# Kernel optimization log

Measured on AMD Instinct MI355X. Metric: run time of the kernel, lower is better.

Reference implementation:

```python
import jax, jax.numpy as jnp
import numpy as np

N_NODES = 2097152  # total nodes
HIDDEN = 64        # feature dim D

def setup_inputs() -> dict:
    key = jax.random.key(0)
    features = jax.random.normal(key, (N_NODES, HIDDEN), dtype=jnp.float32)
    return {"features": features, "n_per_graph": 512}

def reference(features, n_per_graph):
    # features: [N, D]; N = B * n_per_graph (uniform segments)
    N, D = features.shape
    B = N // n_per_graph
    X = features.reshape(B, n_per_graph, D)          # [B, n, D]
    mu = jnp.mean(X, axis=1, keepdims=True)          # [B, 1, D]
    Xc = X - mu                                      # mean-centered
    # per-graph covariance: (Xc^T Xc) / n  -> [B, D, D]
    cov = jnp.einsum('bnd,bne->bde', Xc, Xc) / jnp.asarray(n_per_graph, X.dtype)
    iu0, iu1 = jnp.triu_indices(D)                   # upper triangle incl. diag
    return cov[:, iu0, iu1]                          # [B, D*(D+1)/2]
```

## Files before the change

kernel.cpp:

```cpp
#include <hip/hip_runtime.h>
#include <hip/hip_bf16.h>


#define DD   64
#define NPG  512
#define NIT  (NPG / 32)

typedef __bf16 bf16x8 __attribute__((ext_vector_type(8)));
typedef float  f32x4  __attribute__((ext_vector_type(4)));

__global__ __launch_bounds__(256, 4)
void cov_pool_kernel(const float* __restrict__ X, float* __restrict__ out,
                     int n_graphs) {
  const int lane = threadIdx.x & 63;
  const int w    = threadIdx.x >> 6;
  const long g   = (long)blockIdx.x * 4 + w;
  if (g >= n_graphs) return;

  const int dimq = lane & 15;
  const int kgrp = (lane >> 4) * 8;

  const float* base = X + g * (long)(NPG * DD) + (long)kgrp * DD + dimq;

  f32x4 z = {0.f, 0.f, 0.f, 0.f};
  f32x4 a00=z,a01=z,a02=z,a03=z,a11=z,a12=z,a13=z,a22=z,a23=z,a33=z;
  float cs0=0.f, cs1=0.f, cs2=0.f, cs3=0.f;

  float f0[8], f1[8], f2[8], f3[8];
  #pragma unroll
  for (int j = 0; j < 8; ++j) {
    f0[j] = base[j*DD +  0];
    f1[j] = base[j*DD + 16];
    f2[j] = base[j*DD + 32];
    f3[j] = base[j*DD + 48];
  }

  #pragma unroll 1
  for (int it = 0; it < NIT; ++it) {
    bf16x8 b0, b1, b2, b3;
    #pragma unroll
    for (int j = 0; j < 8; ++j) {
      cs0 += f0[j]; b0[j] = (__bf16)f0[j];
      cs1 += f1[j]; b1[j] = (__bf16)f1[j];
      cs2 += f2[j]; b2[j] = (__bf16)f2[j];
      cs3 += f3[j]; b3[j] = (__bf16)f3[j];
    }
    if (it + 1 < NIT) {
      const float* p = base + (long)(it + 1) * 32 * DD;
      #pragma unroll
      for (int j = 0; j < 8; ++j) {
        f0[j] = p[j*DD +  0];
        f1[j] = p[j*DD + 16];
        f2[j] = p[j*DD + 32];
        f3[j] = p[j*DD + 48];
      }
    }
    a00 = __builtin_amdgcn_mfma_f32_16x16x32_bf16(b0, b0, a00, 0, 0, 0);
    a01 = __builtin_amdgcn_mfma_f32_16x16x32_bf16(b0, b1, a01, 0, 0, 0);
    a02 = __builtin_amdgcn_mfma_f32_16x16x32_bf16(b0, b2, a02, 0, 0, 0);
    a03 = __builtin_amdgcn_mfma_f32_16x16x32_bf16(b0, b3, a03, 0, 0, 0);
    a11 = __builtin_amdgcn_mfma_f32_16x16x32_bf16(b1, b1, a11, 0, 0, 0);
    a12 = __builtin_amdgcn_mfma_f32_16x16x32_bf16(b1, b2, a12, 0, 0, 0);
    a13 = __builtin_amdgcn_mfma_f32_16x16x32_bf16(b1, b3, a13, 0, 0, 0);
    a22 = __builtin_amdgcn_mfma_f32_16x16x32_bf16(b2, b2, a22, 0, 0, 0);
    a23 = __builtin_amdgcn_mfma_f32_16x16x32_bf16(b2, b3, a23, 0, 0, 0);
    a33 = __builtin_amdgcn_mfma_f32_16x16x32_bf16(b3, b3, a33, 0, 0, 0);
  }

  cs0 += __shfl_xor(cs0, 16, 64); cs0 += __shfl_xor(cs0, 32, 64);
  cs1 += __shfl_xor(cs1, 16, 64); cs1 += __shfl_xor(cs1, 32, 64);
  cs2 += __shfl_xor(cs2, 16, 64); cs2 += __shfl_xor(cs2, 32, 64);
  cs3 += __shfl_xor(cs3, 16, 64); cs3 += __shfl_xor(cs3, 32, 64);
  const float inv_n = 1.f / NPG;
  const float mu0 = cs0 * inv_n;
  const float mu1 = cs1 * inv_n;
  const float mu2 = cs2 * inv_n;
  const float mu3 = cs3 * inv_n;

  const int rl = (lane >> 4) * 4;
  float mur0[4], mur1[4], mur2[4], mur3[4];
  #pragma unroll
  for (int r = 0; r < 4; ++r) {
    mur0[r] = __shfl(mu0, rl + r, 64);
    mur1[r] = __shfl(mu1, rl + r, 64);
    mur2[r] = __shfl(mu2, rl + r, 64);
    mur3[r] = __shfl(mu3, rl + r, 64);
  }

  float* og = out + g * 2080L;
  auto wtile = [&](int tr, int tc, const f32x4& A, const float* MR, float MC,
                   bool diag) {
    const int j = tc * 16 + dimq;
    #pragma unroll
    for (int r = 0; r < 4; ++r) {
      const int i = tr * 16 + rl + r;
      if (!diag || j >= i) {
        og[i * DD - (i * (i - 1)) / 2 + (j - i)] = A[r] * inv_n - MR[r] * MC;
      }
    }
  };
  wtile(0, 0, a00, mur0, mu0, true);
  wtile(0, 1, a01, mur0, mu1, false);
  wtile(0, 2, a02, mur0, mu2, false);
  wtile(0, 3, a03, mur0, mu3, false);
  wtile(1, 1, a11, mur1, mu1, true);
  wtile(1, 2, a12, mur1, mu2, false);
  wtile(1, 3, a13, mur1, mu3, false);
  wtile(2, 2, a22, mur2, mu2, true);
  wtile(2, 3, a23, mur2, mu3, false);
  wtile(3, 3, a33, mur3, mu3, true);
}

extern "C" void kernel_launch(void* const* d_in, const int* in_sizes, int n_in,
                              void* d_out, int out_size, void* d_ws, size_t ws_size,
                              hipStream_t stream) {
  const float* X = (const float*)d_in[0];
  float* out = (float*)d_out;
  const int N = in_sizes[0] / DD;
  const int B = N / NPG;
  cov_pool_kernel<<<dim3((B + 3) / 4), dim3(256), 0, stream>>>(X, out, B);
}
```

Baseline: 116.7 us.

## Compute column sums via MFMA with ones vector and split prefetch halves

Replaces the per-lane FP32 column-sum accumulation and the shuffle reduction with four extra MFMA ops that multiply a ones vector by the bf16 tiles, so the matrix core produces the column sums directly. The prefetch is also split into two halves so conversion of one half can overlap loading the next. This removes VALU adds and cross-lane shuffles, but the means now come from bf16-rounded values instead of FP32, which lowers their accuracy and adds 40% more MFMA work per iteration.

Result: slower. 142.8 us (+22.3%).

```diff
diff --git a/kernel.cpp b/kernel.cpp
--- a/kernel.cpp
+++ b/kernel.cpp
@@ -24,37 +24,55 @@
 
   f32x4 z = {0.f, 0.f, 0.f, 0.f};
   f32x4 a00=z,a01=z,a02=z,a03=z,a11=z,a12=z,a13=z,a22=z,a23=z,a33=z;
-  float cs0=0.f, cs1=0.f, cs2=0.f, cs3=0.f;
+  f32x4 am0=z,am1=z,am2=z,am3=z;
 
-  float f0[8], f1[8], f2[8], f3[8];
+  bf16x8 ones;
   #pragma unroll
-  for (int j = 0; j < 8; ++j) {
-    f0[j] = base[j*DD +  0];
-    f1[j] = base[j*DD + 16];
-    f2[j] = base[j*DD + 32];
-    f3[j] = base[j*DD + 48];
-  }
+  for (int j = 0; j < 8; ++j) ones[j] = (__bf16)1.0f;
+
+  float fA[4][4], fB[4][4];
+  #pragma unroll
+  for (int t = 0; t < 4; ++t)
+    #pragma unroll
+    for (int j = 0; j < 4; ++j) {
+      fA[t][j] = base[j * DD + 16 * t];
+      fB[t][j] = base[(4 + j) * DD + 16 * t];
+    }
 
   #pragma unroll 1
   for (int it = 0; it < NIT; ++it) {
+    const float* p = base + (long)(it + 1) * 32 * DD;
     bf16x8 b0, b1, b2, b3;
     #pragma unroll
-    for (int j = 0; j < 8; ++j) {
-      cs0 += f0[j]; b0[j] = (__bf16)f0[j];
-      cs1 += f1[j]; b1[j] = (__bf16)f1[j];
-      cs2 += f2[j]; b2[j] = (__bf16)f2[j];
-      cs3 += f3[j]; b3[j] = (__bf16)f3[j];
+    for (int j = 0; j < 4; ++j) {
+      b0[j] = (__bf16)fA[0][j];
+      b1[j] = (__bf16)fA[1][j];
+      b2[j] = (__bf16)fA[2][j];
+      b3[j] = (__bf16)fA[3][j];
     }
     if (it + 1 < NIT) {
-      const float* p = base + (long)(it + 1) * 32 * DD;
       #pragma unroll
-      for (int j = 0; j < 8; ++j) {
-        f0[j] = p[j*DD +  0];
-        f1[j] = p[j*DD + 16];
-        f2[j] = p[j*DD + 32];
-        f3[j] = p[j*DD + 48];
-      }
+      for (int t = 0; t < 4; ++t)
+        #pragma unroll
+        for (int j = 0; j < 4; ++j) fA[t][j] = p[j * DD + 16 * t];
     }
+    #pragma unroll
+    for (int j = 0; j < 4; ++j) {
+      b0[4 + j] = (__bf16)fB[0][j];
+      b1[4 + j] = (__bf16)fB[1][j];
+      b2[4 + j] = (__bf16)fB[2][j];
+      b3[4 + j] = (__bf16)fB[3][j];
+    }
+    if (it + 1 < NIT) {
+      #pragma unroll
+      for (int t = 0; t < 4; ++t)
+        #pragma unroll
+        for (int j = 0; j < 4; ++j) fB[t][j] = p[(4 + j) * DD + 16 * t];
+    }
+    am0 = __builtin_amdgcn_mfma_f32_16x16x32_bf16(ones, b0, am0, 0, 0, 0);
+    am1 = __builtin_amdgcn_mfma_f32_16x16x32_bf16(ones, b1, am1, 0, 0, 0);
+    am2 = __builtin_amdgcn_mfma_f32_16x16x32_bf16(ones, b2, am2, 0, 0, 0);
+    am3 = __builtin_amdgcn_mfma_f32_16x16x32_bf16(ones, b3, am3, 0, 0, 0);
     a00 = __builtin_amdgcn_mfma_f32_16x16x32_bf16(b0, b0, a00, 0, 0, 0);
     a01 = __builtin_amdgcn_mfma_f32_16x16x32_bf16(b0, b1, a01, 0, 0, 0);
     a02 = __builtin_amdgcn_mfma_f32_16x16x32_bf16(b0, b2, a02, 0, 0, 0);
@@ -67,15 +85,11 @@
     a33 = __builtin_amdgcn_mfma_f32_16x16x32_bf16(b3, b3, a33, 0, 0, 0);
   }
 
-  cs0 += __shfl_xor(cs0, 16, 64); cs0 += __shfl_xor(cs0, 32, 64);
-  cs1 += __shfl_xor(cs1, 16, 64); cs1 += __shfl_xor(cs1, 32, 64);
-  cs2 += __shfl_xor(cs2, 16, 64); cs2 += __shfl_xor(cs2, 32, 64);
-  cs3 += __shfl_xor(cs3, 16, 64); cs3 += __shfl_xor(cs3, 32, 64);
   const float inv_n = 1.f / NPG;
-  const float mu0 = cs0 * inv_n;
-  const float mu1 = cs1 * inv_n;
-  const float mu2 = cs2 * inv_n;
-  const float mu3 = cs3 * inv_n;
+  const float mu0 = am0[0] * inv_n;
+  const float mu1 = am1[0] * inv_n;
+  const float mu2 = am2[0] * inv_n;
+  const float mu3 = am3[0] * inv_n;
 
   const int rl = (lane >> 4) * 4;
   float mur0[4], mur1[4], mur2[4], mur3[4];
```
